# Optimization experiments

Measured on AMD Instinct MI355X. Metric: run time of the kernel, lower is better.

The kernel has to match this reference:

```python
import jax, jax.numpy as jnp
import numpy as np

D_MODEL = 2048
NUM_HEADS = 16
HEAD_DIM = D_MODEL // NUM_HEADS
D_FF = 8192
EPS = 1e-6


def rmsnorm(x, w):
    return x * jax.lax.rsqrt(jnp.mean(x * x, axis=-1, keepdims=True) + EPS) * w


def setup_inputs() -> dict:
    key = jax.random.key(0)
    ks = jax.random.split(key, 8)
    B, S, D = 2, 2048, D_MODEL
    s = lambda d: 1.0 / np.sqrt(d)
    return {
        "x": jax.random.normal(ks[0], (B, S, D), dtype=jnp.float32),
        "w_qkv": jax.random.normal(ks[1], (D, 3 * D), dtype=jnp.float32) * s(D),
        "w_out": jax.random.normal(ks[2], (D, D), dtype=jnp.float32) * s(D),
        "w1": jax.random.normal(ks[3], (D, D_FF), dtype=jnp.float32) * s(D),
        "w2": jax.random.normal(ks[4], (D_FF, D), dtype=jnp.float32) * s(D_FF),
        "w3": jax.random.normal(ks[5], (D, D_FF), dtype=jnp.float32) * s(D),
        "g1": jnp.ones((D,), dtype=jnp.float32),
        "g2": jnp.ones((D,), dtype=jnp.float32),
    }


def attention(x, w_qkv, w_out):
    B, S, D = x.shape
    H, Hd = NUM_HEADS, HEAD_DIM
    qkv = (x @ w_qkv).reshape(B, S, 3, H, Hd)
    q = qkv[:, :, 0].transpose(0, 2, 1, 3)  # [B,H,S,Hd]
    k = qkv[:, :, 1].transpose(0, 2, 1, 3)
    v = qkv[:, :, 2].transpose(0, 2, 1, 3)
    scale = Hd ** -0.5
    attn = jnp.einsum("bhqd,bhkd->bhqk", q, k) * scale
    causal = jnp.tril(jnp.ones((S, S), dtype=bool))
    attn = jnp.where(causal, attn, -jnp.inf)
    attn = jax.nn.softmax(attn, axis=-1)
    out = jnp.einsum("bhqk,bhkd->bhqd", attn, v)
    out = out.transpose(0, 2, 1, 3).reshape(B, S, D)
    return out @ w_out


def ffn(x, w1, w2, w3):
    return (jax.nn.silu(x @ w1) * (x @ w3)) @ w2


def reference(x, w_qkv, w_out, w1, w2, w3, g1, g2):
    x = x + attention(rmsnorm(x, g1), w_qkv, w_out)
    return x + ffn(rmsnorm(x, g2), w1, w2, w3)
```

## Files before the change

### kernel.cpp

```cpp
#include <hip/hip_runtime.h>
#include <cstdint>
#include <cstddef>

typedef __bf16 bf16x8 __attribute__((ext_vector_type(8)));
typedef __bf16 bf16x4 __attribute__((ext_vector_type(4)));
typedef float f32x4 __attribute__((ext_vector_type(4)));

__device__ __forceinline__ void gl_lds16(const void* g, void* l) {
  __builtin_amdgcn_global_load_lds(
      (const __attribute__((address_space(1))) void*)g,
      (__attribute__((address_space(3))) void*)l, 16, 0, 0);
}

__global__ __launch_bounds__(256) void wconv_t_k(const float* __restrict__ W,
                                                 __bf16* __restrict__ WT,
                                                 int K, int N) {
  __shared__ float tile[64][68];
  const int c0 = blockIdx.x * 64, r0 = blockIdx.y * 64;
  const int t = threadIdx.x;
  const int lr = t >> 4;
  const int lc = (t & 15) * 4;
#pragma unroll
  for (int i = 0; i < 4; ++i) {
    float4 v = *(const float4*)&W[(size_t)(r0 + lr + i * 16) * N + c0 + lc];
    *(float4*)&tile[lr + i * 16][lc] = v;
  }
  __syncthreads();
  const int cr = t >> 4, kb = (t & 15) * 4;
#pragma unroll
  for (int j = 0; j < 4; ++j) {
    const int c = cr + j * 16;
    bf16x4 o;
    o[0] = (__bf16)tile[kb + 0][c];
    o[1] = (__bf16)tile[kb + 1][c];
    o[2] = (__bf16)tile[kb + 2][c];
    o[3] = (__bf16)tile[kb + 3][c];
    *(bf16x4*)&WT[(size_t)(c0 + c) * K + r0 + kb] = o;
  }
}

__global__ __launch_bounds__(256) void rmsnorm_k(const float* __restrict__ x,
                                                 const float* __restrict__ g,
                                                 __bf16* __restrict__ out) {
  constexpr int D = 2048;
  const int row = blockIdx.x, t = threadIdx.x;
  const float4* xr = (const float4*)(x + (size_t)row * D);
  float4 a = xr[t * 2], b2 = xr[t * 2 + 1];
  float ss = a.x * a.x + a.y * a.y + a.z * a.z + a.w * a.w +
             b2.x * b2.x + b2.y * b2.y + b2.z * b2.z + b2.w * b2.w;
#pragma unroll
  for (int d = 1; d < 64; d <<= 1) ss += __shfl_xor(ss, d, 64);
  __shared__ float red[4];
  if ((t & 63) == 0) red[t >> 6] = ss;
  __syncthreads();
  float rs = rsqrtf((red[0] + red[1] + red[2] + red[3]) * (1.f / D) + 1e-6f);
  const float4* gr = (const float4*)g;
  float4 ga = gr[t * 2], gb = gr[t * 2 + 1];
  bf16x8 o8;
  o8[0] = (__bf16)(a.x * rs * ga.x);
  o8[1] = (__bf16)(a.y * rs * ga.y);
  o8[2] = (__bf16)(a.z * rs * ga.z);
  o8[3] = (__bf16)(a.w * rs * ga.w);
  o8[4] = (__bf16)(b2.x * rs * gb.x);
  o8[5] = (__bf16)(b2.y * rs * gb.y);
  o8[6] = (__bf16)(b2.z * rs * gb.z);
  o8[7] = (__bf16)(b2.w * rs * gb.w);
  *(bf16x8*)(out + (size_t)row * D + t * 8) = o8;
}

__global__ __launch_bounds__(256) void addrms_k(const float* __restrict__ p0,
                                                const float* __restrict__ p1,
                                                const float* __restrict__ res,
                                                const float* __restrict__ g,
                                                float* __restrict__ hout,
                                                __bf16* __restrict__ xnout) {
  constexpr int D = 2048;
  const int row = blockIdx.x, t = threadIdx.x;
  const size_t base = (size_t)row * D;
  float4 h[2];
#pragma unroll
  for (int j = 0; j < 2; ++j) {
    float4 a = ((const float4*)(p0 + base))[t * 2 + j];
    float4 b = ((const float4*)(p1 + base))[t * 2 + j];
    float4 c = ((const float4*)(res + base))[t * 2 + j];
    h[j].x = a.x + b.x + c.x; h[j].y = a.y + b.y + c.y;
    h[j].z = a.z + b.z + c.z; h[j].w = a.w + b.w + c.w;
    ((float4*)(hout + base))[t * 2 + j] = h[j];
  }
  float ss = h[0].x * h[0].x + h[0].y * h[0].y + h[0].z * h[0].z + h[0].w * h[0].w +
             h[1].x * h[1].x + h[1].y * h[1].y + h[1].z * h[1].z + h[1].w * h[1].w;
#pragma unroll
  for (int d = 1; d < 64; d <<= 1) ss += __shfl_xor(ss, d, 64);
  __shared__ float red[4];
  if ((t & 63) == 0) red[t >> 6] = ss;
  __syncthreads();
  float rs = rsqrtf((red[0] + red[1] + red[2] + red[3]) * (1.f / D) + 1e-6f);
  const float4* gr = (const float4*)g;
  float4 ga = gr[t * 2], gb = gr[t * 2 + 1];
  bf16x8 o8;
  o8[0] = (__bf16)(h[0].x * rs * ga.x);
  o8[1] = (__bf16)(h[0].y * rs * ga.y);
  o8[2] = (__bf16)(h[0].z * rs * ga.z);
  o8[3] = (__bf16)(h[0].w * rs * ga.w);
  o8[4] = (__bf16)(h[1].x * rs * gb.x);
  o8[5] = (__bf16)(h[1].y * rs * gb.y);
  o8[6] = (__bf16)(h[1].z * rs * gb.z);
  o8[7] = (__bf16)(h[1].w * rs * gb.w);
  *(bf16x8*)(xnout + base + t * 8) = o8;
}

__global__ __launch_bounds__(256) void addred_k(const float* __restrict__ p0,
                                                const float* __restrict__ p1,
                                                const float* __restrict__ res,
                                                float* __restrict__ out, int n4) {
  int i = blockIdx.x * 256 + threadIdx.x;
  const int stride = gridDim.x * 256;
  for (; i < n4; i += stride) {
    float4 a = ((const float4*)p0)[i];
    float4 b = ((const float4*)p1)[i];
    float4 c = ((const float4*)res)[i];
    float4 o = {a.x + b.x + c.x, a.y + b.y + c.y, a.z + b.z + c.z, a.w + b.w + c.w};
    ((float4*)out)[i] = o;
  }
}

#define RD_A(BUF, HALF) do {                                        \
  const __bf16* aT_ = &As[BUF][0] + aoff + (HALF) * 4096;           \
  _Pragma("unroll")                                                 \
  for (int mi = 0; mi < 4; ++mi) {                                  \
    Ar[mi][0] = *(const bf16x8*)(aT_ + mi * 1024 + k0off);          \
    Ar[mi][1] = *(const bf16x8*)(aT_ + mi * 1024 + k1off);          \
  } } while (0)

#define RD_B(BUF, NH) do {                                          \
  const __bf16* bT_ = &Bs[BUF][0] + boff + (NH) * 2048;             \
  _Pragma("unroll")                                                 \
  for (int ni = 0; ni < 2; ++ni) {                                  \
    Br[NH][ni][0] = *(const bf16x8*)(bT_ + ni * 1024 + k0off);      \
    Br[NH][ni][1] = *(const bf16x8*)(bT_ + ni * 1024 + k1off);      \
  } } while (0)

#define MQ(MH, NH) do {                                             \
  __builtin_amdgcn_s_setprio(1);                                    \
  _Pragma("unroll")                                                 \
  for (int mi = 0; mi < 4; ++mi) {                                  \
    _Pragma("unroll")                                               \
    for (int ni = 0; ni < 2; ++ni) {                                \
      f32x4& a_ = acc[(MH) * 4 + mi][(NH) * 2 + ni];                \
      a_ = __builtin_amdgcn_mfma_f32_16x16x32_bf16(Ar[mi][0], Br[NH][ni][0], a_, 0, 0, 0); \
      a_ = __builtin_amdgcn_mfma_f32_16x16x32_bf16(Ar[mi][1], Br[NH][ni][1], a_, 0, 0, 0); \
    } }                                                             \
  __builtin_amdgcn_s_setprio(0);                                    \
} while (0)

#define PEND(VM) do {                                               \
  __builtin_amdgcn_sched_barrier(0);                                \
  asm volatile("s_waitcnt vmcnt(" #VM ")" ::: "memory");            \
  __builtin_amdgcn_s_barrier();                                     \
  __builtin_amdgcn_sched_barrier(0);                                \
} while (0)

#define PEND_NOVM() do {                                            \
  __builtin_amdgcn_sched_barrier(0);                                \
  __builtin_amdgcn_s_barrier();                                     \
  __builtin_amdgcn_sched_barrier(0);                                \
} while (0)

#define KTILE(BUF, STG0, STG1, STG2, STG3, END0, END1, END2, END3) do { \
  RD_A(BUF, 0); RD_B(BUF, 0); RD_B(BUF, 1);                         \
  MQ(0, 0); STG0; END0;                                             \
  MQ(0, 1); RD_A(BUF, 1); STG1; END1;                               \
  MQ(1, 1); STG2; END2;                                             \
  MQ(1, 0); STG3; END3;                                             \
} while (0)

template <int MODE>
__global__ __launch_bounds__(512, 2) void gemm8_k(
    const __bf16* __restrict__ A, const __bf16* __restrict__ BT,
    const float* __restrict__ res, const __bf16* __restrict__ aux,
    void* __restrict__ Cout, int M, int N, int K, int lda, int cswz) {
  __shared__ alignas(16) __bf16 As[2][256 * 64];
  __shared__ alignas(16) __bf16 Bs[2][256 * 64];
  const int tid = threadIdx.x;
  const int lane = tid & 63, w = tid >> 6;
  const int wm = w >> 2, wn = w & 3;
  const int l15 = lane & 15, l16 = lane >> 4;

  const int nbx = gridDim.x, nby = gridDim.y;
  const int nwg = nbx * nby;
  const int bid = blockIdx.y * nbx + blockIdx.x;
  const int swz = (bid & 7) * (nwg >> 3) + (bid >> 3);
  int bx, by;
  if (cswz) { by = swz % nby; bx = swz / nby; }
  else      { bx = swz % nbx; by = swz / nbx; }
  const int m0 = by * 256, n0 = bx * 256;
  const int nkt = K >> 6;

  float* CoutF = (float*)Cout;
  if constexpr (MODE == 4) {
    const int z = blockIdx.z;
    A += (size_t)z * K;
    BT += (size_t)z * K;
    CoutF += (size_t)z * M * N;
  }

  const int srow = tid >> 3;
  const int scole = ((tid & 7) * 8) ^ ((srow & 7) << 3);
  const int brow_i = ((tid >> 8) << 6) + ((tid >> 3) & 31);

  auto stgA = [&](int t, int h) {
    if (t < nkt) {
      char* dst = (char*)(&As[t & 1][0]) + h * 8192 + tid * 16;
      const __bf16* src = A + (size_t)(m0 + h * 64 + srow) * lda + t * 64 + scole;
      gl_lds16(src, dst);
      gl_lds16(src + (size_t)128 * lda, dst + 16384);
    }
  };
  auto stgB = [&](int t, int h) {
    if (t < nkt) {
      const int r = h * 32 + brow_i;
      char* dst = (char*)(&Bs[t & 1][0]) + r * 128 + (tid & 7) * 16;
      const __bf16* src = BT + (size_t)(n0 + r) * lda + t * 64 + scole;
      gl_lds16(src, dst);
      gl_lds16(src + (size_t)128 * lda, dst + 16384);
    }
  };

  const int rswz = (l15 & 7) << 3;
  const int k0off = (l16 * 8) ^ rswz;
  const int k1off = (32 + l16 * 8) ^ rswz;
  const int aoff = (wm * 128 + l15) * 64;
  const int boff = (wn * 64 + l15) * 64;

  f32x4 acc[8][4] = {};
  bf16x8 Ar[4][2], Br[2][2][2];

  stgA(0, 0); stgB(0, 0); stgB(0, 1); stgA(0, 1);
  stgA(1, 0); stgB(1, 0);
  asm volatile("s_waitcnt vmcnt(6)" ::: "memory");
  __builtin_amdgcn_s_barrier();
  __builtin_amdgcn_sched_barrier(0);

  int t = 0;
  for (; t + 3 < nkt; t += 2) {
    KTILE(0, stgB(t + 1, 1), stgA(t + 1, 1), stgA(t + 2, 0), stgB(t + 2, 0),
          PEND(6), PEND_NOVM(), PEND_NOVM(), PEND(6));
    KTILE(1, stgB(t + 2, 1), stgA(t + 2, 1), stgA(t + 3, 0), stgB(t + 3, 0),
          PEND(6), PEND_NOVM(), PEND_NOVM(), PEND(6));
  }
  KTILE(0, stgB(t + 1, 1), stgA(t + 1, 1), (void)0, (void)0,
        PEND(6), PEND_NOVM(), PEND_NOVM(), PEND(2));
  KTILE(1, (void)0, (void)0, (void)0, (void)0,
        PEND(0), PEND_NOVM(), PEND_NOVM(), (void)0);

#pragma unroll
  for (int m = 0; m < 8; ++m) {
    const int rowb = m0 + wm * 128 + m * 16 + l16 * 4;
#pragma unroll
    for (int n = 0; n < 4; ++n) {
      const int col = n0 + wn * 64 + n * 16 + l15;
#pragma unroll
      for (int r = 0; r < 4; ++r) {
        const size_t idx = (size_t)(rowb + r) * N + col;
        float v = acc[m][n][r];
        if constexpr (MODE == 1) {
          CoutF[idx] = v + res[idx];
        } else if constexpr (MODE == 2) {
          float s = v / (1.f + __expf(-v));
          ((__bf16*)Cout)[idx] = (__bf16)s;
        } else if constexpr (MODE == 3) {
          ((__bf16*)Cout)[idx] = (__bf16)(v * (float)aux[idx]);
        } else if constexpr (MODE == 4) {
          CoutF[idx] = v;
        } else {
          ((__bf16*)Cout)[idx] = (__bf16)v;
        }
      }
    }
  }
}

__global__ __launch_bounds__(256) void vtrans_k(const __bf16* __restrict__ qkv,
                                                __bf16* __restrict__ VT) {
  constexpr int S = 2048;
  __shared__ __bf16 tile[64][65];
  const int s0 = blockIdx.x * 64, d0 = blockIdx.y * 64;
  const int bh = blockIdx.z, b = bh >> 4, h = bh & 15;
  const int tx = threadIdx.x & 63, ty = threadIdx.x >> 6;
  const size_t vbase = ((size_t)b * S * 3 + 2) * 2048 + h * 128;
#pragma unroll
  for (int i = 0; i < 16; ++i) {
    int s = ty + i * 4;
    tile[s][tx] = qkv[vbase + (size_t)(s0 + s) * 6144 + d0 + tx];
  }
  __syncthreads();
  const size_t obase = ((size_t)bh * 128 + d0) * S + s0;
#pragma unroll
  for (int i = 0; i < 16; ++i) {
    int d = ty + i * 4;
    VT[obase + (size_t)d * S + tx] = tile[tx][d];
  }
}

__global__ __launch_bounds__(512) void attn_k(const __bf16* __restrict__ qkv,
                                              const __bf16* __restrict__ VT,
                                              __bf16* __restrict__ out) {
  constexpr int S = 2048;
  const int bid = blockIdx.x;
  const int bh = (bid & 7) * 4 + ((bid >> 3) & 3);
  const int qb = 15 - (bid >> 5);
  const int b = bh >> 4, h = bh & 15;
  const int q0 = qb * 128;
  const int tid = threadIdx.x, lane = tid & 63, w = tid >> 6;
  const int l15 = lane & 15, l16 = lane >> 4;

  __shared__ __bf16 Ks[64 * 128];
  __shared__ __bf16 Vs[128 * 64];
  __shared__ __bf16 Ps[8][16 * 72];

  const size_t qbase = (size_t)b * S * 6144 + h * 128;
  const size_t kbase = qbase + 2048;
  const size_t vtbase = (size_t)bh * 128 * 2048;

  bf16x8 qf[4];
  {
    const __bf16* qp = qkv + qbase + (size_t)(q0 + w * 16 + l15) * 6144 + l16 * 8;
#pragma unroll
    for (int kc = 0; kc < 4; ++kc) qf[kc] = *(const bf16x8*)(qp + kc * 32);
  }

  f32x4 o[8] = {};
  float mrow[4] = {-1e30f, -1e30f, -1e30f, -1e30f};
  float lrow[4] = {0.f, 0.f, 0.f, 0.f};
  const float sm = 0.08838834764831845f * 1.4426950408889634f;

  int ksrow[2], kscol[2], vsrow[2], vscol[2];
#pragma unroll
  for (int c = 0; c < 2; ++c) {
    int P = (c * 512 + tid) * 16;
    int kr = P >> 8;
    ksrow[c] = kr;
    kscol[c] = ((P & 255) ^ ((kr & 7) << 4)) >> 1;
    int vr = P >> 7;
    vsrow[c] = vr;
    vscol[c] = ((P & 127) ^ ((vr & 7) << 4)) >> 1;
  }
  const int fswz = (l15 & 7) << 3;
  const int qrow_abs = q0 + w * 16 + l16 * 4;

#pragma unroll
  for (int c = 0; c < 2; ++c) {
    int e = (c * 512 + tid) * 8;
    gl_lds16(qkv + kbase + (size_t)ksrow[c] * 6144 + kscol[c], &Ks[e]);
    gl_lds16(VT + vtbase + (size_t)vsrow[c] * 2048 + vscol[c], &Vs[e]);
  }

  const int ntk = 2 * qb + 2;
  for (int kt = 0; kt < ntk; ++kt) {
    const int k0 = kt * 64;
    __syncthreads();

    bf16x8 kreg[2], vreg[2];
    const bool pf = kt + 1 < ntk;
    if (pf) {
      const int kn = k0 + 64;
#pragma unroll
      for (int c = 0; c < 2; ++c)
        kreg[c] = *(const bf16x8*)(qkv + kbase + (size_t)(kn + ksrow[c]) * 6144 + kscol[c]);
#pragma unroll
      for (int c = 0; c < 2; ++c)
        vreg[c] = *(const bf16x8*)(VT + vtbase + (size_t)vsrow[c] * 2048 + kn + vscol[c]);
    }

    f32x4 s4[4];
    __builtin_amdgcn_s_setprio(1);
#pragma unroll
    for (int f = 0; f < 4; ++f) {
      f32x4 accs = {};
#pragma unroll
      for (int kc = 0; kc < 4; ++kc) {
        bf16x8 kf = *(const bf16x8*)&Ks[(f * 16 + l15) * 128 + ((kc * 32 + l16 * 8) ^ fswz)];
        accs = __builtin_amdgcn_mfma_f32_16x16x32_bf16(qf[kc], kf, accs, 0, 0, 0);
      }
      s4[f] = accs;
    }
    __builtin_amdgcn_s_setprio(0);

    float pm[4] = {-1e30f, -1e30f, -1e30f, -1e30f};
    float pvv[4][4];
#pragma unroll
    for (int f = 0; f < 4; ++f) {
      const int key = k0 + f * 16 + l15;
#pragma unroll
      for (int r = 0; r < 4; ++r) {
        float s = s4[f][r] * sm;
        if (key > qrow_abs + r) s = -1e30f;
        pvv[f][r] = s;
        pm[r] = fmaxf(pm[r], s);
      }
    }
#pragma unroll
    for (int d = 1; d < 16; d <<= 1) {
#pragma unroll
      for (int r = 0; r < 4; ++r) pm[r] = fmaxf(pm[r], __shfl_xor(pm[r], d, 64));
    }
    float fac[4], ts[4];
#pragma unroll
    for (int r = 0; r < 4; ++r) {
      float mn = fmaxf(mrow[r], pm[r]);
      fac[r] = exp2f(mrow[r] - mn);
      mrow[r] = mn;
      ts[r] = 0.f;
    }
#pragma unroll
    for (int f = 0; f < 4; ++f) {
#pragma unroll
      for (int r = 0; r < 4; ++r) {
        float p = exp2f(pvv[f][r] - mrow[r]);
        ts[r] += p;
        Ps[w][(l16 * 4 + r) * 72 + f * 16 + l15] = (__bf16)p;
      }
    }
#pragma unroll
    for (int d = 1; d < 16; d <<= 1) {
#pragma unroll
      for (int r = 0; r < 4; ++r) ts[r] += __shfl_xor(ts[r], d, 64);
    }
#pragma unroll
    for (int r = 0; r < 4; ++r) lrow[r] = lrow[r] * fac[r] + ts[r];
#pragma unroll
    for (int n = 0; n < 8; ++n) {
      o[n][0] *= fac[0];
      o[n][1] *= fac[1];
      o[n][2] *= fac[2];
      o[n][3] *= fac[3];
    }
    __builtin_amdgcn_s_setprio(1);
#pragma unroll
    for (int kc = 0; kc < 2; ++kc) {
      bf16x8 pf2 = *(const bf16x8*)&Ps[w][l15 * 72 + kc * 32 + l16 * 8];
#pragma unroll
      for (int n = 0; n < 8; ++n) {
        bf16x8 vf = *(const bf16x8*)&Vs[(n * 16 + l15) * 64 + ((kc * 32 + l16 * 8) ^ fswz)];
        o[n] = __builtin_amdgcn_mfma_f32_16x16x32_bf16(pf2, vf, o[n], 0, 0, 0);
      }
    }
    __builtin_amdgcn_s_setprio(0);
    __syncthreads();

    if (pf) {
#pragma unroll
      for (int c = 0; c < 2; ++c) *(bf16x8*)&Ks[(c * 512 + tid) * 8] = kreg[c];
#pragma unroll
      for (int c = 0; c < 2; ++c) *(bf16x8*)&Vs[(c * 512 + tid) * 8] = vreg[c];
    }
  }

  const int orow = b * S + q0 + w * 16 + l16 * 4;
#pragma unroll
  for (int r = 0; r < 4; ++r) {
    const float inv = 1.f / lrow[r];
#pragma unroll
    for (int n = 0; n < 8; ++n)
      out[(size_t)(orow + r) * 2048 + h * 128 + n * 16 + l15] = (__bf16)(o[n][r] * inv);
  }
}

extern "C" void kernel_launch(void* const* d_in, const int* in_sizes, int n_in,
                              void* d_out, int out_size, void* d_ws, size_t ws_size,
                              hipStream_t stream) {
  (void)in_sizes; (void)n_in; (void)out_size; (void)ws_size;
  const float* x = (const float*)d_in[0];
  const float* w_qkv = (const float*)d_in[1];
  const float* w_out = (const float*)d_in[2];
  const float* w1 = (const float*)d_in[3];
  const float* w2 = (const float*)d_in[4];
  const float* w3 = (const float*)d_in[5];
  const float* g1 = (const float*)d_in[6];
  const float* g2 = (const float*)d_in[7];
  char* ws = (char*)d_ws;

  constexpr int Mr = 4096, D = 2048, DFF = 8192, TD = 6144;

  __bf16* wqkvT = (__bf16*)(ws + 0);
  __bf16* w1T   = (__bf16*)(ws + 0);
  __bf16* woutT = (__bf16*)(ws + 33554432);
  __bf16* qkvb  = (__bf16*)(ws + 41943040);
  __bf16* w3T   = (__bf16*)(ws + 41943040);
  __bf16* w2T   = (__bf16*)(ws + 75497472);
  __bf16* VTb   = (__bf16*)(ws + 92274688);
  __bf16* xn    = (__bf16*)(ws + 109051904);
  __bf16* attn  = (__bf16*)(ws + 125829120);
  float*  hbuf  = (float*)(ws + 142606336);
  __bf16* gbuf  = (__bf16*)(ws + 176160768);
  float*  pO    = (float*)(ws + 176160768);
  float*  pW0   = (float*)(ws + 0);

  wconv_t_k<<<dim3(TD / 64, D / 64), 256, 0, stream>>>(w_qkv, wqkvT, D, TD);
  wconv_t_k<<<dim3(D / 64, D / 64), 256, 0, stream>>>(w_out, woutT, D, D);
  rmsnorm_k<<<Mr, 256, 0, stream>>>(x, g1, xn);
  gemm8_k<0><<<dim3(TD / 256, Mr / 256), 512, 0, stream>>>(xn, wqkvT, nullptr, nullptr, qkvb, Mr, TD, D, D, 1);
  vtrans_k<<<dim3(32, 2, 32), 256, 0, stream>>>(qkvb, VTb);
  attn_k<<<512, 512, 0, stream>>>(qkvb, VTb, attn);
  gemm8_k<4><<<dim3(D / 256, Mr / 256, 2), 512, 0, stream>>>(attn, woutT, nullptr, nullptr, pO, Mr, D, D / 2, D, 0);
  addrms_k<<<Mr, 256, 0, stream>>>(pO, pO + (size_t)Mr * D, x, g2, hbuf, xn);
  wconv_t_k<<<dim3(DFF / 64, D / 64), 256, 0, stream>>>(w1, w1T, D, DFF);
  wconv_t_k<<<dim3(DFF / 64, D / 64), 256, 0, stream>>>(w3, w3T, D, DFF);
  wconv_t_k<<<dim3(D / 64, DFF / 64), 256, 0, stream>>>(w2, w2T, DFF, D);
  gemm8_k<2><<<dim3(DFF / 256, Mr / 256), 512, 0, stream>>>(xn, w1T, nullptr, nullptr, gbuf, Mr, DFF, D, D, 1);
  gemm8_k<3><<<dim3(DFF / 256, Mr / 256), 512, 0, stream>>>(xn, w3T, nullptr, gbuf, gbuf, Mr, DFF, D, D, 1);
  gemm8_k<4><<<dim3(D / 256, Mr / 256, 2), 512, 0, stream>>>(gbuf, w2T, nullptr, nullptr, pW0, Mr, D, DFF / 2, DFF, 0);
  addred_k<<<2048, 256, 0, stream>>>(pW0, pW0 + (size_t)Mr * D, hbuf, (float*)d_out, Mr * D / 4);
}
```

Before: 729.8 us.

## Restructure GEMM k-tile pipeline to two barriers per tile with batched prefetch

Reorganizes the double-buffered bf16 GEMM main loop so each k-tile uses two barrier gates instead of four. All four MFMA quadrants run under one high-priority region, and the next tile's A/B stages are issued together mid-tile. The aim is to cut barrier and synchronisation overhead and lengthen uninterrupted MFMA runs. The cost is a different vmcnt accounting and less fine-grained interleaving of loads with compute, which could expose memory latency or introduce races if the counts are wrong.

```diff
diff --git a/kernel.cpp b/kernel.cpp
--- a/kernel.cpp
+++ b/kernel.cpp
@@ -140,8 +140,7 @@
     Br[NH][ni][1] = *(const bf16x8*)(bT_ + ni * 1024 + k1off);      \
   } } while (0)
 
-#define MQ(MH, NH) do {                                             \
-  __builtin_amdgcn_s_setprio(1);                                    \
+#define MQ0(MH, NH) do {                                            \
   _Pragma("unroll")                                                 \
   for (int mi = 0; mi < 4; ++mi) {                                  \
     _Pragma("unroll")                                               \
@@ -149,29 +148,26 @@
       f32x4& a_ = acc[(MH) * 4 + mi][(NH) * 2 + ni];                \
       a_ = __builtin_amdgcn_mfma_f32_16x16x32_bf16(Ar[mi][0], Br[NH][ni][0], a_, 0, 0, 0); \
       a_ = __builtin_amdgcn_mfma_f32_16x16x32_bf16(Ar[mi][1], Br[NH][ni][1], a_, 0, 0, 0); \
-    } }                                                             \
-  __builtin_amdgcn_s_setprio(0);                                    \
-} while (0)
-
-#define PEND(VM) do {                                               \
+    } } } while (0)
+
+#define GATE(VM) do {                                               \
   __builtin_amdgcn_sched_barrier(0);                                \
   asm volatile("s_waitcnt vmcnt(" #VM ")" ::: "memory");            \
   __builtin_amdgcn_s_barrier();                                     \
   __builtin_amdgcn_sched_barrier(0);                                \
 } while (0)
 
-#define PEND_NOVM() do {                                            \
-  __builtin_amdgcn_sched_barrier(0);                                \
-  __builtin_amdgcn_s_barrier();                                     \
-  __builtin_amdgcn_sched_barrier(0);                                \
-} while (0)
-
-#define KTILE(BUF, STG0, STG1, STG2, STG3, END0, END1, END2, END3) do { \
+#define KT3(BUF, PRESTG, POSTSTG, GATEA, GATEEND) do {              \
   RD_A(BUF, 0); RD_B(BUF, 0); RD_B(BUF, 1);                         \
-  MQ(0, 0); STG0; END0;                                             \
-  MQ(0, 1); RD_A(BUF, 1); STG1; END1;                               \
-  MQ(1, 1); STG2; END2;                                             \
-  MQ(1, 0); STG3; END3;                                             \
+  PRESTG;                                                           \
+  GATEA;                                                            \
+  __builtin_amdgcn_s_setprio(1);                                    \
+  MQ0(0, 0); MQ0(0, 1);                                             \
+  RD_A(BUF, 1);                                                     \
+  POSTSTG;                                                          \
+  MQ0(1, 1); MQ0(1, 0);                                             \
+  __builtin_amdgcn_s_setprio(0);                                    \
+  GATEEND;                                                          \
 } while (0)
 
 template <int MODE>
@@ -235,23 +231,23 @@
   f32x4 acc[8][4] = {};
   bf16x8 Ar[4][2], Br[2][2][2];
 
-  stgA(0, 0); stgB(0, 0); stgB(0, 1); stgA(0, 1);
-  stgA(1, 0); stgB(1, 0);
-  asm volatile("s_waitcnt vmcnt(6)" ::: "memory");
+  stgA(0, 0); stgB(0, 0); stgB(0, 1);
+  stgA(0, 1); stgA(1, 0); stgB(1, 0); stgB(1, 1);
+  asm volatile("s_waitcnt vmcnt(8)" ::: "memory");
   __builtin_amdgcn_s_barrier();
   __builtin_amdgcn_sched_barrier(0);
 
   int t = 0;
   for (; t + 3 < nkt; t += 2) {
-    KTILE(0, stgB(t + 1, 1), stgA(t + 1, 1), stgA(t + 2, 0), stgB(t + 2, 0),
-          PEND(6), PEND_NOVM(), PEND_NOVM(), PEND(6));
-    KTILE(1, stgB(t + 2, 1), stgA(t + 2, 1), stgA(t + 3, 0), stgB(t + 3, 0),
-          PEND(6), PEND_NOVM(), PEND_NOVM(), PEND(6));
-  }
-  KTILE(0, stgB(t + 1, 1), stgA(t + 1, 1), (void)0, (void)0,
-        PEND(6), PEND_NOVM(), PEND_NOVM(), PEND(2));
-  KTILE(1, (void)0, (void)0, (void)0, (void)0,
-        PEND(0), PEND_NOVM(), PEND_NOVM(), (void)0);
+    KT3(0, stgA(t + 1, 1),
+        { stgA(t + 2, 0); stgB(t + 2, 0); stgB(t + 2, 1); },
+        GATE(6), GATE(8));
+    KT3(1, stgA(t + 2, 1),
+        { stgA(t + 3, 0); stgB(t + 3, 0); stgB(t + 3, 1); },
+        GATE(6), GATE(8));
+  }
+  KT3(0, stgA(t + 1, 1), (void)0, GATE(6), GATE(2));
+  KT3(1, (void)0, (void)0, GATE(0), (void)0);
 
 #pragma unroll
   for (int m = 0; m < 8; ++m) {
```

Measured after the change: 724.3 us, median of 3. About the same (-0.8%).
